# Performance work log

Measured on AMD Instinct MI355X. Metric: run time of the kernel, lower is better.

## Reference

```python
import jax, jax.numpy as jnp
import numpy as np
import math

D_MODEL = 256
NUM_HEADS = 8
D_HEAD = D_MODEL // NUM_HEADS


def setup_inputs() -> dict:
    key = jax.random.key(0)
    k1, k2, k3, k4, k5 = jax.random.split(key, 5)
    B, T, N = 8, 32, 256
    x = jax.random.normal(k1, (B, T, N, D_MODEL), dtype=jnp.float32)
    boxes_in_flat = jax.random.uniform(k2, (B * T * N, 4), dtype=jnp.float32)
    s = 1.0 / math.sqrt(D_MODEL)
    W_Q = jax.random.uniform(k3, (D_MODEL, D_MODEL), jnp.float32, -s, s)
    W_K = jax.random.uniform(k4, (D_MODEL, D_MODEL), jnp.float32, -s, s)
    W_V = jax.random.uniform(k5, (D_MODEL, D_MODEL), jnp.float32, -s, s)
    return {"x": x, "boxes_in_flat": boxes_in_flat, "W_Q": W_Q, "W_K": W_K, "W_V": W_V}


def reference(x, boxes_in_flat, W_Q, W_K, W_V):
    # x: [B, T, N, D]; boxes_in_flat is unused by the original forward.
    B, T, N, D = x.shape
    H, dh = NUM_HEADS, D_HEAD
    # Temporal attention pooling: softmax over T, weighted sum over T.
    t_w = jax.nn.softmax(x, axis=1)              # [B,T,N,D]
    TAtt = jnp.sum(x * t_w, axis=1)              # [B,N,D] (original tiles this over T; identical values)
    # QKV projections (nn.Linear without bias: y = x @ W^T).
    Q = (x @ W_Q.T).reshape(B, T, N, H, dh)      # [B,T,N,H,dh]
    K = (TAtt @ W_K.T).reshape(B, N, H, dh)      # [B,N,H,dh]
    V = (TAtt @ W_V.T).reshape(B, N, H, dh)      # [B,N,H,dh]
    # ReLU-scored attention with added self-loop (identity), no softmax.
    A = jnp.einsum('btnhd,bmhd->bthnm', Q, K) / jnp.sqrt(jnp.asarray(dh, x.dtype))
    A = jax.nn.relu(A) + jnp.eye(N, dtype=x.dtype)  # [B,T,H,N,N]
    out = jnp.einsum('bthnm,bmhd->btnhd', A, V)     # [B,T,N,H,dh]
    return out.reshape(B, T, N, H * dh)
```

## Files before the change

### kernel.cpp

```cpp
#include <hip/hip_runtime.h>
#include <hip/hip_bf16.h>

#define BB 8
#define TT 32
#define NN 256
#define DD 256
#define HH 8
#define DH 32

typedef __attribute__((ext_vector_type(8))) short short8v;
typedef __attribute__((ext_vector_type(4))) float f32x4;
typedef __attribute__((ext_vector_type(4))) unsigned int u32x4;

static __device__ __forceinline__ unsigned short f2bfu(float f) {
    __hip_bfloat16 h = __float2bfloat16(f);
    unsigned short u;
    __builtin_memcpy(&u, &h, 2);
    return u;
}
static __device__ __forceinline__ unsigned int pkbf(float a, float b) {
    float2 f2; f2.x = a; f2.y = b;
    __hip_bfloat162 h2 = __float22bfloat162_rn(f2);
    unsigned int u;
    __builtin_memcpy(&u, &h2, 4);
    return u;
}

__global__ __launch_bounds__(256) void wfrag_kernel(const float* __restrict__ Wq,
                                                    const float* __restrict__ Wk,
                                                    const float* __restrict__ Wv,
                                                    short* __restrict__ Wf) {
    int bid = blockIdx.x;
    int mat = bid >> 4, ctile = bid & 15;
    const float* W = (mat == 0) ? Wq : (mat == 1) ? Wk : Wv;
    short* out = Wf + (size_t)mat * (16 * 8 * 64 * 8) + (size_t)ctile * (8 * 64 * 8);
    int tid = threadIdx.x;
    int kc = tid >> 5, kg = (tid >> 3) & 3, j = tid & 7;
#pragma unroll
    for (int i = 0; i < 16; ++i) {
        float v = W[(size_t)(ctile * 16 + i) * DD + tid];
        int lane = i | (kg << 4);
        out[((size_t)kc * 64 + lane) * 8 + j] = (short)f2bfu(v);
    }
}

__global__ __launch_bounds__(256) void tatt_kernel(const float* __restrict__ x,
                                                   float* __restrict__ tatt) {
    int gid = blockIdx.x * 256 + threadIdx.x;
    int b = gid >> 16;
    int rem = gid & 0xFFFF;
    const float* xp = x + (size_t)b * TT * NN * DD + rem;
    float vals[TT];
    float mx = -3.0e38f;
#pragma unroll
    for (int t = 0; t < TT; ++t) {
        vals[t] = xp[(size_t)t * (NN * DD)];
        mx = fmaxf(mx, vals[t]);
    }
    float se = 0.f, wsum = 0.f;
#pragma unroll
    for (int t = 0; t < TT; ++t) {
        float e = __expf(vals[t] - mx);
        se += e;
        wsum += e * vals[t];
    }
    tatt[gid] = wsum / se;
}

__global__ __launch_bounds__(256) void kv_kernel(const float* __restrict__ tatt,
                                                 const short* __restrict__ Wkf,
                                                 const short* __restrict__ Wvf,
                                                 short* __restrict__ Kf,
                                                 short* __restrict__ Vf) {
    __shared__ short Xb[64][264];
    int row0 = blockIdx.x * 64;
    int tid = threadIdx.x;

#pragma unroll
    for (int i = 0; i < 16; ++i) {
        int f = i * 256 + tid;
        int rr = f >> 6;
        int c4 = f & 63;
        float4 xv = *(const float4*)(tatt + (size_t)(row0 + rr) * DD + c4 * 4);
        short4 sv;
        sv.x = (short)f2bfu(xv.x);
        sv.y = (short)f2bfu(xv.y);
        sv.z = (short)f2bfu(xv.z);
        sv.w = (short)f2bfu(xv.w);
        *(short4*)&Xb[rr][c4 * 4] = sv;
    }
    __syncthreads();

    int w = tid >> 6, l = tid & 63;
    int lg = l >> 4, lr = l & 15;
    const f32x4 zero = {0.f, 0.f, 0.f, 0.f};

#pragma unroll
    for (int mat = 0; mat < 2; ++mat) {
        const short* Wfm = mat ? Wvf : Wkf;
#pragma unroll
        for (int ct = 0; ct < 4; ++ct) {
            int c = ct * 64 + w * 16 + lr;
            int ctile = ct * 4 + w;
            short8v bf[8];
#pragma unroll
            for (int kc = 0; kc < 8; ++kc)
                bf[kc] = *(const short8v*)(Wfm + (((size_t)ctile * 8 + kc) * 64 + l) * 8);
            int h = c >> 5, j = c & 31;
#pragma unroll
            for (int rt4 = 0; rt4 < 4; ++rt4) {
                f32x4 acc = zero;
#pragma unroll
                for (int kc = 0; kc < 8; ++kc) {
                    short8v a = *(const short8v*)&Xb[rt4 * 16 + lr][kc * 32 + lg * 8];
                    acc = __builtin_amdgcn_mfma_f32_16x16x32_bf16(a, bf[kc], acc, 0, 0, 0);
                }
#pragma unroll
                for (int r = 0; r < 4; ++r) {
                    int row = row0 + rt4 * 16 + lg * 4 + r;
                    int b = row >> 8, n = row & 255;
                    if (mat == 0) {
                        float val = acc[r] * 0.17677669529663688f;
                        int mt = n >> 4;
                        int laneK = (n & 15) | ((j >> 3) << 4);
                        Kf[((size_t)(b * HH + h) * 16 + mt) * 512 + laneK * 8 + (j & 7)] =
                            (short)f2bfu(val);
                    } else {
                        int mc = n >> 5, grp = (n >> 3) & 3, dt = j >> 4;
                        int laneV = (j & 15) | (grp << 4);
                        Vf[((size_t)(b * HH + h) * 16 + mc * 2 + dt) * 512 + laneV * 8 + (n & 7)] =
                            (short)f2bfu(acc[r]);
                    }
                }
            }
        }
    }
}

__global__ __launch_bounds__(256) void qproj_kernel(const float* __restrict__ x,
                                                    const short* __restrict__ Wqf,
                                                    short* __restrict__ Qb) {
    __shared__ short Xb[64][264];
    int row0 = blockIdx.x * 64;
    int tid = threadIdx.x;

#pragma unroll
    for (int i = 0; i < 16; ++i) {
        int f = i * 256 + tid;
        int rr = f >> 6;
        int c4 = f & 63;
        float4 xv = *(const float4*)(x + (size_t)(row0 + rr) * DD + c4 * 4);
        short4 sv;
        sv.x = (short)f2bfu(xv.x);
        sv.y = (short)f2bfu(xv.y);
        sv.z = (short)f2bfu(xv.z);
        sv.w = (short)f2bfu(xv.w);
        *(short4*)&Xb[rr][c4 * 4] = sv;
    }
    __syncthreads();

    int w = tid >> 6, l = tid & 63;
    int lg = l >> 4, lr = l & 15;
    const f32x4 zero = {0.f, 0.f, 0.f, 0.f};

#pragma unroll
    for (int ct = 0; ct < 4; ++ct) {
        int c = ct * 64 + w * 16 + lr;
        int ctile = ct * 4 + w;
        short8v bf[8];
#pragma unroll
        for (int kc = 0; kc < 8; ++kc)
            bf[kc] = *(const short8v*)(Wqf + (((size_t)ctile * 8 + kc) * 64 + l) * 8);
        int h = c >> 5, jj = c & 31;
#pragma unroll
        for (int rt4 = 0; rt4 < 4; ++rt4) {
            f32x4 acc = zero;
#pragma unroll
            for (int kc = 0; kc < 8; ++kc) {
                short8v a = *(const short8v*)&Xb[rt4 * 16 + lr][kc * 32 + lg * 8];
                acc = __builtin_amdgcn_mfma_f32_16x16x32_bf16(a, bf[kc], acc, 0, 0, 0);
            }
#pragma unroll
            for (int r = 0; r < 4; ++r) {
                int row = row0 + rt4 * 16 + lg * 4 + r;
                int b = row >> 13;
                int t = (row >> 8) & 31;
                int n = row & 255;
                Qb[((((size_t)b * TT + t) * HH + h) * NN + n) * DH + jj] = (short)f2bfu(acc[r]);
            }
        }
    }
}

__global__ __launch_bounds__(256) void attn_kernel(const short* __restrict__ Qb,
                                                   const short* __restrict__ Kf,
                                                   const short* __restrict__ Vf,
                                                   float* __restrict__ out) {
    __shared__ unsigned int Plds[4][8][260];
    int bid = blockIdx.x;
    int h = bid & 7;
    int t = (bid >> 3) & 31;
    int b = bid >> 8;
    int tid = threadIdx.x;
    int w = tid >> 6, l = tid & 63;
    int lg = l >> 4, lr = l & 15;

    const short* kbase = Kf + (size_t)(b * HH + h) * 16 * 512 + l * 8;
    const short* vbase = Vf + (size_t)(b * HH + h) * 16 * 512 + l * 8;
    short8v kfr[16], vfr[16];
#pragma unroll
    for (int i = 0; i < 16; ++i) {
        kfr[i] = *(const short8v*)(kbase + i * 512);
        vfr[i] = *(const short8v*)(vbase + i * 512);
    }

    const short* qbase = Qb + (((size_t)(b * TT + t) * HH + h) * NN + w * 64) * DH;
    const f32x4 zero = {0.f, 0.f, 0.f, 0.f};
    unsigned int (*P)[260] = Plds[w];
    unsigned int sel = (l & 1) ? 0x07060302u : 0x05040100u;
    int qp = lr >> 1;

    for (int qt = 0; qt < 4; ++qt) {
        short8v qf = *(const short8v*)(qbase + (qt * 16 + lr) * DH + lg * 8);
        int qb2 = w * 4 + qt;

#pragma unroll
        for (int mt = 0; mt < 16; ++mt) {
            f32x4 s = __builtin_amdgcn_mfma_f32_16x16x32_bf16(qf, kfr[mt], zero, 0, 0, 0);
            float p0 = fmaxf(s[0], 0.f);
            float p1 = fmaxf(s[1], 0.f);
            float p2 = fmaxf(s[2], 0.f);
            float p3 = fmaxf(s[3], 0.f);
            if (mt == qb2) {
                if (lr == lg * 4 + 0) p0 += 1.f;
                if (lr == lg * 4 + 1) p1 += 1.f;
                if (lr == lg * 4 + 2) p2 += 1.f;
                if (lr == lg * 4 + 3) p3 += 1.f;
            }
            P[2 * lg + 0][mt * 16 + lr] = pkbf(p0, p1);
            P[2 * lg + 1][mt * 16 + lr] = pkbf(p2, p3);
        }

        f32x4 o0 = zero, o1 = zero;
#pragma unroll
        for (int mc = 0; mc < 8; ++mc) {
            const unsigned int* pp = &P[qp][mc * 32 + lg * 8];
            u32x4 ra = *(const u32x4*)pp;
            u32x4 rb = *(const u32x4*)(pp + 4);
            union { unsigned int u[4]; short8v s; } pu;
            pu.u[0] = __builtin_amdgcn_perm(ra[1], ra[0], sel);
            pu.u[1] = __builtin_amdgcn_perm(ra[3], ra[2], sel);
            pu.u[2] = __builtin_amdgcn_perm(rb[1], rb[0], sel);
            pu.u[3] = __builtin_amdgcn_perm(rb[3], rb[2], sel);
            short8v pa = pu.s;
            o0 = __builtin_amdgcn_mfma_f32_16x16x32_bf16(pa, vfr[mc * 2 + 0], o0, 0, 0, 0);
            o1 = __builtin_amdgcn_mfma_f32_16x16x32_bf16(pa, vfr[mc * 2 + 1], o1, 0, 0, 0);
        }

#pragma unroll
        for (int r = 0; r < 4; ++r) {
            int n = w * 64 + qt * 16 + lg * 4 + r;
            float* op = out + ((size_t)(b * TT + t) * NN + n) * DD + h * DH + lr;
            op[0] = o0[r];
            op[16] = o1[r];
        }
    }
}

extern "C" void kernel_launch(void* const* d_in, const int* in_sizes, int n_in,
                              void* d_out, int out_size, void* d_ws, size_t ws_size,
                              hipStream_t stream) {
    (void)in_sizes; (void)n_in; (void)out_size; (void)ws_size;
    const float* x  = (const float*)d_in[0];
    const float* Wq = (const float*)d_in[2];
    const float* Wk = (const float*)d_in[3];
    const float* Wv = (const float*)d_in[4];
    float* out = (float*)d_out;

    char* base = (char*)d_ws;
    float* tatt = (float*)base;
    short* Kfp = (short*)(base + (size_t)2 * 1024 * 1024);
    short* Vfp = (short*)(base + (size_t)3 * 1024 * 1024);
    short* Qbp = (short*)(base + (size_t)4 * 1024 * 1024);
    short* Wf  = (short*)(base + (size_t)36 * 1024 * 1024);
    short* Wqf = Wf;
    short* Wkf = Wf + (size_t)16 * 8 * 64 * 8;
    short* Wvf = Wkf + (size_t)16 * 8 * 64 * 8;

    wfrag_kernel<<<48, 256, 0, stream>>>(Wq, Wk, Wv, Wf);
    tatt_kernel<<<(BB * NN * DD) / 256, 256, 0, stream>>>(x, tatt);
    kv_kernel<<<BB * NN / 64, 256, 0, stream>>>(tatt, Wkf, Wvf, Kfp, Vfp);
    qproj_kernel<<<BB * TT * NN / 64, 256, 0, stream>>>(x, Wqf, Qbp);
    attn_kernel<<<BB * TT * HH, 256, 0, stream>>>(Qbp, Kfp, Vfp, out);
}
```

Measured before the change: 172.8 us.

## Switch attention to 32x32 MFMA with register-resident P via permlane32 swap

Rewrites the attention kernel to use 32x32x16 bf16 MFMAs, computing the transposed score tile K·Q so that the ReLU'd probabilities can be repacked in registers with permlane32_swap and fed directly as the A operand of the P·V MFMA. This removes the LDS round trip for P and its perm shuffles. Q, K and V are rewritten by the projection kernels into matching 32x32 fragment layouts. K and V fragments are now streamed per key tile instead of preloaded into registers, and launch bounds request higher occupancy. Output stores become strided column writes per lane, which may be less coalesced.

```diff
diff --git a/kernel.cpp b/kernel.cpp
--- a/kernel.cpp
+++ b/kernel.cpp
@@ -10,7 +10,8 @@
 
 typedef __attribute__((ext_vector_type(8))) short short8v;
 typedef __attribute__((ext_vector_type(4))) float f32x4;
-typedef __attribute__((ext_vector_type(4))) unsigned int u32x4;
+typedef __attribute__((ext_vector_type(16))) float f32x16;
+typedef __attribute__((ext_vector_type(2))) unsigned int u32x2;
 
 static __device__ __forceinline__ unsigned short f2bfu(float f) {
     __hip_bfloat16 h = __float2bfloat16(f);
@@ -106,7 +107,7 @@
 #pragma unroll
             for (int kc = 0; kc < 8; ++kc)
                 bf[kc] = *(const short8v*)(Wfm + (((size_t)ctile * 8 + kc) * 64 + l) * 8);
-            int h = c >> 5, j = c & 31;
+            int h = c >> 5, kap = c & 31;
 #pragma unroll
             for (int rt4 = 0; rt4 < 4; ++rt4) {
                 f32x4 acc = zero;
@@ -121,15 +122,14 @@
                     int b = row >> 8, n = row & 255;
                     if (mat == 0) {
                         float val = acc[r] * 0.17677669529663688f;
-                        int mt = n >> 4;
-                        int laneK = (n & 15) | ((j >> 3) << 4);
-                        Kf[((size_t)(b * HH + h) * 16 + mt) * 512 + laneK * 8 + (j & 7)] =
-                            (short)f2bfu(val);
+                        size_t o = ((((size_t)(b * HH + h) * 8 + (n >> 5)) * 2 + (kap >> 4)) * 64
+                                    + (n & 31) + 32 * ((kap >> 3) & 1)) * 8 + (kap & 7);
+                        Kf[o] = (short)f2bfu(val);
                     } else {
-                        int mc = n >> 5, grp = (n >> 3) & 3, dt = j >> 4;
-                        int laneV = (j & 15) | (grp << 4);
-                        Vf[((size_t)(b * HH + h) * 16 + mc * 2 + dt) * 512 + laneV * 8 + (n & 7)] =
-                            (short)f2bfu(acc[r]);
+                        int d = kap;
+                        size_t o = ((((size_t)(b * HH + h) * 8 + (n >> 5)) * 2 + ((n >> 4) & 1)) * 64
+                                    + d + 32 * ((n >> 3) & 1)) * 8 + (n & 7);
+                        Vf[o] = (short)f2bfu(acc[r]);
                     }
                 }
             }
@@ -171,7 +171,7 @@
 #pragma unroll
         for (int kc = 0; kc < 8; ++kc)
             bf[kc] = *(const short8v*)(Wqf + (((size_t)ctile * 8 + kc) * 64 + l) * 8);
-        int h = c >> 5, jj = c & 31;
+        int h = c >> 5, kap = c & 31;
 #pragma unroll
         for (int rt4 = 0; rt4 < 4; ++rt4) {
             f32x4 acc = zero;
@@ -186,84 +186,87 @@
                 int b = row >> 13;
                 int t = (row >> 8) & 31;
                 int n = row & 255;
-                Qb[((((size_t)b * TT + t) * HH + h) * NN + n) * DH + jj] = (short)f2bfu(acc[r]);
+                size_t o = (((((size_t)(b * TT + t) * HH + h) * 8 + (n >> 5)) * 2 + (kap >> 4)) * 64
+                            + (n & 31) + 32 * ((kap >> 3) & 1)) * 8 + (kap & 7);
+                Qb[o] = (short)f2bfu(acc[r]);
             }
         }
     }
 }
 
-__global__ __launch_bounds__(256) void attn_kernel(const short* __restrict__ Qb,
-                                                   const short* __restrict__ Kf,
-                                                   const short* __restrict__ Vf,
-                                                   float* __restrict__ out) {
-    __shared__ unsigned int Plds[4][8][260];
+__global__ __launch_bounds__(256, 4) void attn_kernel(const short* __restrict__ Qf,
+                                                      const short* __restrict__ Kf,
+                                                      const short* __restrict__ Vf,
+                                                      float* __restrict__ out) {
     int bid = blockIdx.x;
     int h = bid & 7;
     int t = (bid >> 3) & 31;
     int b = bid >> 8;
     int tid = threadIdx.x;
     int w = tid >> 6, l = tid & 63;
-    int lg = l >> 4, lr = l & 15;
-
-    const short* kbase = Kf + (size_t)(b * HH + h) * 16 * 512 + l * 8;
-    const short* vbase = Vf + (size_t)(b * HH + h) * 16 * 512 + l * 8;
-    short8v kfr[16], vfr[16];
-#pragma unroll
-    for (int i = 0; i < 16; ++i) {
-        kfr[i] = *(const short8v*)(kbase + i * 512);
-        vfr[i] = *(const short8v*)(vbase + i * 512);
-    }
-
-    const short* qbase = Qb + (((size_t)(b * TT + t) * HH + h) * NN + w * 64) * DH;
-    const f32x4 zero = {0.f, 0.f, 0.f, 0.f};
-    unsigned int (*P)[260] = Plds[w];
-    unsigned int sel = (l & 1) ? 0x07060302u : 0x05040100u;
-    int qp = lr >> 1;
-
-    for (int qt = 0; qt < 4; ++qt) {
-        short8v qf = *(const short8v*)(qbase + (qt * 16 + lr) * DH + lg * 8);
-        int qb2 = w * 4 + qt;
-
-#pragma unroll
-        for (int mt = 0; mt < 16; ++mt) {
-            f32x4 s = __builtin_amdgcn_mfma_f32_16x16x32_bf16(qf, kfr[mt], zero, 0, 0, 0);
-            float p0 = fmaxf(s[0], 0.f);
-            float p1 = fmaxf(s[1], 0.f);
-            float p2 = fmaxf(s[2], 0.f);
-            float p3 = fmaxf(s[3], 0.f);
-            if (mt == qb2) {
-                if (lr == lg * 4 + 0) p0 += 1.f;
-                if (lr == lg * 4 + 1) p1 += 1.f;
-                if (lr == lg * 4 + 2) p2 += 1.f;
-                if (lr == lg * 4 + 3) p3 += 1.f;
-            }
-            P[2 * lg + 0][mt * 16 + lr] = pkbf(p0, p1);
-            P[2 * lg + 1][mt * 16 + lr] = pkbf(p2, p3);
+    int pos = l & 31, hi = l >> 5;
+
+    const short8v* qp = (const short8v*)Qf + ((size_t)bid * 8 + 2 * w) * 2 * 64 + l;
+    short8v qf00 = qp[0];
+    short8v qf01 = qp[64];
+    short8v qf10 = qp[128];
+    short8v qf11 = qp[192];
+
+    const short8v* kp = (const short8v*)Kf + (size_t)(b * HH + h) * 16 * 64 + l;
+    const short8v* vp = (const short8v*)Vf + (size_t)(b * HH + h) * 16 * 64 + l;
+
+    const f32x16 z16 = {};
+    f32x16 o0 = z16, o1 = z16;
+
+#pragma unroll 2
+    for (int mt = 0; mt < 8; ++mt) {
+        short8v kf0 = kp[mt * 128];
+        short8v kf1 = kp[mt * 128 + 64];
+        short8v vf0 = vp[mt * 128];
+        short8v vf1 = vp[mt * 128 + 64];
+#pragma unroll
+        for (int qi = 0; qi < 2; ++qi) {
+            short8v qa = qi ? qf10 : qf00;
+            short8v qb = qi ? qf11 : qf01;
+            f32x16 p = __builtin_amdgcn_mfma_f32_32x32x16_bf16(kf0, qa, z16, 0, 0, 0);
+            p = __builtin_amdgcn_mfma_f32_32x32x16_bf16(kf1, qb, p, 0, 0, 0);
+#pragma unroll
+            for (int r = 0; r < 16; ++r) p[r] = fmaxf(p[r], 0.f);
+            if (mt == 2 * w + qi) {
+#pragma unroll
+                for (int r = 0; r < 16; ++r) {
+                    int mloc = (r & 3) + 8 * (r >> 2) + 4 * hi;
+                    if (mloc == pos) p[r] += 1.f;
+                }
+            }
+#pragma unroll
+            for (int c = 0; c < 2; ++c) {
+                unsigned int A0 = pkbf(p[8 * c + 0], p[8 * c + 1]);
+                unsigned int A1 = pkbf(p[8 * c + 2], p[8 * c + 3]);
+                unsigned int B0 = pkbf(p[8 * c + 4], p[8 * c + 5]);
+                unsigned int B1 = pkbf(p[8 * c + 6], p[8 * c + 7]);
+                u32x2 s0 = __builtin_amdgcn_permlane32_swap(A0, B0, false, false);
+                u32x2 s1 = __builtin_amdgcn_permlane32_swap(A1, B1, false, false);
+                union { unsigned int u[4]; short8v s; } pa;
+                pa.u[0] = s0[0];
+                pa.u[1] = s1[0];
+                pa.u[2] = s0[1];
+                pa.u[3] = s1[1];
+                short8v vv = c ? vf1 : vf0;
+                if (qi == 0)
+                    o0 = __builtin_amdgcn_mfma_f32_32x32x16_bf16(pa.s, vv, o0, 0, 0, 0);
+                else
+                    o1 = __builtin_amdgcn_mfma_f32_32x32x16_bf16(pa.s, vv, o1, 0, 0, 0);
+            }
         }
-
-        f32x4 o0 = zero, o1 = zero;
-#pragma unroll
-        for (int mc = 0; mc < 8; ++mc) {
-            const unsigned int* pp = &P[qp][mc * 32 + lg * 8];
-            u32x4 ra = *(const u32x4*)pp;
-            u32x4 rb = *(const u32x4*)(pp + 4);
-            union { unsigned int u[4]; short8v s; } pu;
-            pu.u[0] = __builtin_amdgcn_perm(ra[1], ra[0], sel);
-            pu.u[1] = __builtin_amdgcn_perm(ra[3], ra[2], sel);
-            pu.u[2] = __builtin_amdgcn_perm(rb[1], rb[0], sel);
-            pu.u[3] = __builtin_amdgcn_perm(rb[3], rb[2], sel);
-            short8v pa = pu.s;
-            o0 = __builtin_amdgcn_mfma_f32_16x16x32_bf16(pa, vfr[mc * 2 + 0], o0, 0, 0, 0);
-            o1 = __builtin_amdgcn_mfma_f32_16x16x32_bf16(pa, vfr[mc * 2 + 1], o1, 0, 0, 0);
-        }
-
-#pragma unroll
-        for (int r = 0; r < 4; ++r) {
-            int n = w * 64 + qt * 16 + lg * 4 + r;
-            float* op = out + ((size_t)(b * TT + t) * NN + n) * DD + h * DH + lr;
-            op[0] = o0[r];
-            op[16] = o1[r];
-        }
+    }
+
+    float* ob = out + ((size_t)(b * TT + t) * NN) * DD + h * DH + pos;
+#pragma unroll
+    for (int r = 0; r < 16; ++r) {
+        int mloc = (r & 3) + 8 * (r >> 2) + 4 * hi;
+        ob[(size_t)((2 * w + 0) * 32 + mloc) * DD] = o0[r];
+        ob[(size_t)((2 * w + 1) * 32 + mloc) * DD] = o1[r];
     }
 }
 
```

New measurement: 180.3 us. 1.04x slower.
